# Performance work log

Hardware: AMD Instinct MI355X
Metric: run time of the kernel (lower is better)

The kernel has to match this reference:

```python
import jax, jax.numpy as jnp
import numpy as np

H_DIM = 64
GRID = 8
NS = 2.0  # neighborhood_size
S = 256   # number of sequences (scenes)
P = 64    # pedestrians per sequence
EPS = 1e-5


def setup_inputs() -> dict:
    key = jax.random.key(0)
    k = jax.random.split(key, 6)
    N = S * P
    G = GRID * GRID
    h_states = jax.random.normal(k[0], (1, N, H_DIM), jnp.float32)
    end_pos = jax.random.normal(k[1], (N, 2), jnp.float32)
    starts = (jnp.arange(S, dtype=jnp.int32) * P)
    seq_start_end = jnp.stack([starts, starts + P], axis=1)  # (S, 2)
    # mlp_pool: Linear(G*H_DIM -> H_DIM) + BatchNorm1d + ReLU
    W = jax.random.normal(k[2], (G * H_DIM, H_DIM), jnp.float32) / np.sqrt(G * H_DIM)
    b = jnp.zeros((H_DIM,), jnp.float32)
    gamma = jnp.ones((H_DIM,), jnp.float32)
    beta = jnp.zeros((H_DIM,), jnp.float32)
    return {"h_states": h_states, "seq_start_end": seq_start_end, "end_pos": end_pos,
            "W": W, "b": b, "gamma": gamma, "beta": beta}


def reference(h_states, seq_start_end, end_pos, W, b, gamma, beta):
    nseq = seq_start_end.shape[0]          # S (static)
    N = end_pos.shape[0]
    Hd = h_states.shape[-1]
    nped = N // nseq                       # P (static; equal-length sequences)
    G = GRID * GRID
    half = NS / 2.0

    h = h_states.reshape(N, Hd).reshape(nseq, nped, Hd)     # (S, P, H)
    pos = end_pos.reshape(nseq, nped, 2)                    # (S, P, 2)

    # bounds per center pedestrian i
    tl_x = pos[..., 0] - half   # (S, P)
    tl_y = pos[..., 1] + half
    br_x = pos[..., 0] + half
    br_y = pos[..., 1] - half

    # pairwise: axis 1 = center i, axis 2 = other k
    ox = pos[:, None, :, 0]     # (S, 1, P)
    oy = pos[:, None, :, 1]
    cell_x = jnp.floor((ox - tl_x[:, :, None]) / NS * GRID)
    cell_y = jnp.floor((tl_y[:, :, None] - oy) / NS * GRID)
    grid = cell_x + cell_y * GRID                            # (S, P, P)

    oob = ((ox >= br_x[:, :, None]) | (ox <= tl_x[:, :, None]) |
           (oy >= tl_y[:, :, None]) | (oy <= br_y[:, :, None]))
    diag = jnp.eye(nped, dtype=bool)[None]                   # self excluded (within_bound[0::P+1]=1)
    valid = (~oob) & (~diag)

    grid_i = jnp.clip(grid.astype(jnp.int32), 0, G - 1)      # masked entries don't matter
    seq_off = (jnp.arange(nseq, dtype=jnp.int32)[:, None, None] * nped
               + jnp.arange(nped, dtype=jnp.int32)[None, :, None]) * G
    dummy = nseq * nped * G
    ids = jnp.where(valid, seq_off + grid_i, dummy)          # (S, P, P)

    # data for (s, i, k) is hidden of other k (curr_hidden.repeat(num_ped, 1))
    data = jnp.broadcast_to(h[:, None, :, :], (nseq, nped, nped, Hd)).reshape(-1, Hd)
    pooled = jax.ops.segment_sum(data, ids.reshape(-1), num_segments=dummy + 1)[:-1]
    x = pooled.reshape(N, G * Hd)                            # (N, G*H), row i = concat over grid cells

    # mlp_pool: Linear -> BatchNorm1d (train mode, biased var) -> ReLU
    x = x @ W + b
    mu = jnp.mean(x, axis=0)
    var = jnp.mean((x - mu) ** 2, axis=0)
    x = gamma * (x - mu) / jnp.sqrt(var + EPS) + beta
    return jnp.maximum(x, 0.0)
```

## Files before the change

kernel.cpp:

```cpp
#include <hip/hip_runtime.h>
#include <hip/hip_bf16.h>


#define NSEQ 256
#define NTOT (NSEQ*64)
#define EPSV 1e-5f

typedef __attribute__((ext_vector_type(8))) short short8;
typedef __attribute__((ext_vector_type(4))) float f32x4;
typedef unsigned short ushort_t;

__device__ __forceinline__ ushort_t f2b(float f) {
    __hip_bfloat16 h = __float2bfloat16(f);
    return *reinterpret_cast<ushort_t*>(&h);
}
__device__ __forceinline__ int kperm(int k) {
    return ((k >> 5)*2 + ((k & 7) >> 2))*16 + ((k >> 3) & 3)*4 + (k & 3);
}

__global__ __launch_bounds__(256) void sp_transpose(
    const float* __restrict__ W, short* __restrict__ Wt)
{
    __shared__ __align__(16) float Tl[64*68];
    const int b = blockIdx.x, tid = threadIdx.x;
    const float* wg = W + (size_t)b*4096;
    for (int m = 0; m < 4; ++m) {
        int c = m*256 + tid;
        int k = c >> 4, t0 = (c & 15)*4;
        *(f32x4*)(Tl + k*68 + t0) = *(const f32x4*)(wg + k*64 + t0);
    }
    __syncthreads();
    for (int m = 0; m < 2; ++m) {
        int q = m*256 + tid;
        int col = q >> 3, k0 = (q & 7)*8;
        short8 o;
        #pragma unroll
        for (int i2 = 0; i2 < 8; ++i2)
            o[i2] = (short)f2b(Tl[kperm(k0 + i2)*68 + col]);
        *(short8*)(Wt + ((size_t)(b*64 + col)*64 + k0)) = o;
    }
}

#define SM_CM   9216
#define SM_POS  13312
#define SM_RED  17408
#define SM_TOT  19456

__global__ __launch_bounds__(512, 2) void sp_main(
    const float* __restrict__ h, const float* __restrict__ pos,
    const short* __restrict__ Wt, const float* __restrict__ bvec,
    float* __restrict__ X, float* __restrict__ partials)
{
    __shared__ __align__(16) char smem[SM_TOT];
    ushort_t*      Ht = (ushort_t*)(smem);
    unsigned char* cm = (unsigned char*)(smem + SM_CM);
    float*         px = (float*)(smem + SM_POS);
    float*         py = px + 64;

    const int b    = blockIdx.x;
    const int base = b * 64;
    const int tid  = threadIdx.x;
    const int lane = tid & 63, w = tid >> 6;
    const int ln15 = lane & 15, ln4 = lane >> 4;

    if (tid < 64) { px[tid] = pos[(base + tid)*2]; py[tid] = pos[(base + tid)*2 + 1]; }
    for (int m = 0; m < 2; ++m) {
        int c = m*512 + tid;
        int j = c >> 4, t0 = (c & 15)*4;
        f32x4 v = *(const f32x4*)(h + (size_t)(base + j)*64 + t0);
        #pragma unroll
        for (int u = 0; u < 4; ++u) Ht[(t0 + u)*72 + j] = f2b(v[u]);
    }
    __syncthreads();

    for (int m = 0; m < 8; ++m) {
        int p = m*512 + tid;
        int i = p >> 6, j = p & 63;
        unsigned char val = 255;
        if (i != j) {
            float ax = px[i], ay = py[i], ox = px[j], oy = py[j];
            float tlx = ax - 1.0f, tly = ay + 1.0f, brx = ax + 1.0f, bry = ay - 1.0f;
            bool oob = (ox >= brx) | (ox <= tlx) | (oy >= tly) | (oy <= bry);
            if (!oob) {
                int g = (int)(floorf((ox - tlx)*4.0f) + floorf((tly - oy)*4.0f)*8.0f);
                g = g < 0 ? 0 : (g > 63 ? 63 : g);
                val = (unsigned char)g;
            }
        }
        cm[i*64 + j] = val;
    }
    __syncthreads();

    short8 hf2[4][2];
    #pragma unroll
    for (int mt = 0; mt < 4; ++mt)
        #pragma unroll
        for (int kt2 = 0; kt2 < 2; ++kt2)
            hf2[mt][kt2] = *(const short8*)(Ht + (mt*16 + ln15)*72 + kt2*32 + ln4*8);
    unsigned cmv[4][2][2];
    #pragma unroll
    for (int rt = 0; rt < 4; ++rt)
        #pragma unroll
        for (int kt = 0; kt < 2; ++kt) {
            const unsigned* cp = (const unsigned*)(cm + (rt*16 + ln15)*64 + kt*32 + ln4*8);
            cmv[rt][kt][0] = cp[0]; cmv[rt][kt][1] = cp[1];
        }

    f32x4 acc[4][4];
    #pragma unroll
    for (int rt = 0; rt < 4; ++rt)
        #pragma unroll
        for (int nt = 0; nt < 4; ++nt) acc[rt][nt] = (f32x4){0.f,0.f,0.f,0.f};

    for (int c = 0; c < 8; ++c) {
        const int g = w*8 + ((c + b) & 7);
        const short* wg = Wt + (size_t)g*4096;
        short8 bw[2][4];
        #pragma unroll
        for (int kt = 0; kt < 2; ++kt)
            #pragma unroll
            for (int nt = 0; nt < 4; ++nt)
                bw[kt][nt] = *(const short8*)(wg + (nt*16 + ln15)*64 + kt*32 + ln4*8);

        #pragma unroll
        for (int rt = 0; rt < 4; ++rt) {
            short8 sf[2];
            #pragma unroll
            for (int kt = 0; kt < 2; ++kt)
                #pragma unroll
                for (int u = 0; u < 8; ++u) {
                    unsigned byte = ((u < 4 ? cmv[rt][kt][0] >> (8*u)
                                           : cmv[rt][kt][1] >> (8*(u-4))) & 255u);
                    sf[kt][u] = (byte == (unsigned)g) ? (short)0x3F80 : (short)0;
                }
            f32x4 pt[4];
            #pragma unroll
            for (int mt = 0; mt < 4; ++mt) pt[mt] = (f32x4){0.f,0.f,0.f,0.f};
            #pragma unroll
            for (int kt2 = 0; kt2 < 2; ++kt2)
                #pragma unroll
                for (int mt = 0; mt < 4; ++mt)
                    pt[mt] = __builtin_amdgcn_mfma_f32_16x16x32_bf16(hf2[mt][kt2], sf[kt2], pt[mt], 0, 0, 0);
            #pragma unroll
            for (int kt = 0; kt < 2; ++kt) {
                short8 af;
                #pragma unroll
                for (int r = 0; r < 4; ++r) {
                    af[r]     = (short)f2b(pt[2*kt    ][r]);
                    af[4 + r] = (short)f2b(pt[2*kt + 1][r]);
                }
                #pragma unroll
                for (int nt = 0; nt < 4; ++nt)
                    acc[rt][nt] = __builtin_amdgcn_mfma_f32_16x16x32_bf16(af, bw[kt][nt], acc[rt][nt], 0, 0, 0);
            }
        }
    }
    __syncthreads();

    float* Xs = (float*)smem;
    for (int wv = 0; wv < 8; ++wv) {
        if (w == wv) {
            #pragma unroll
            for (int rt = 0; rt < 4; ++rt)
                #pragma unroll
                for (int nt = 0; nt < 4; ++nt)
                    #pragma unroll
                    for (int r = 0; r < 4; ++r) {
                        int row = rt*16 + ln4*4 + r;
                        int col = nt*16 + ln15;
                        if (wv == 0) Xs[row*68 + col]  = acc[rt][nt][r];
                        else         Xs[row*68 + col] += acc[rt][nt][r];
                    }
        }
        __syncthreads();
    }

    {
        const int row = tid >> 3, c0 = (tid & 7)*8;
        float* xg = X + (size_t)(base + row)*64 + c0;
        #pragma unroll
        for (int q = 0; q < 2; ++q) {
            f32x4 v;
            #pragma unroll
            for (int u = 0; u < 4; ++u) v[u] = Xs[row*68 + c0 + q*4 + u] + bvec[c0 + q*4 + u];
            *(f32x4*)(xg + q*4) = v;
        }
    }

    {
        float* red1 = (float*)(smem + SM_RED);
        float* red2 = red1 + 256;
        if (tid < 256) {
            int col = tid & 63, rg = tid >> 6;
            float bc = bvec[col], s1 = 0.f, s2 = 0.f;
            for (int ii = 0; ii < 16; ++ii) {
                float xv = Xs[(rg*16 + ii)*68 + col] + bc;
                s1 += xv; s2 += xv*xv;
            }
            red1[rg*64 + col] = s1;
            red2[rg*64 + col] = s2;
        }
        __syncthreads();
        if (tid < 128) {
            int hs = tid >> 6, c2 = tid & 63;
            const float* r0 = hs ? red2 : red1;
            float v = r0[c2] + r0[64 + c2] + r0[128 + c2] + r0[192 + c2];
            partials[(size_t)b*128 + hs*64 + c2] = v;
        }
    }
}

__global__ __launch_bounds__(256) void sp_finish(
    float* __restrict__ X, const float* __restrict__ partials,
    const float* __restrict__ gamma, const float* __restrict__ beta)
{
    __shared__ float sp0[128], sp1[128];
    __shared__ float scale[64], shift[64];
    const int b = blockIdx.x, tid = threadIdx.x;

    {
        const int slot = tid & 127, hb = tid >> 7;
        float v = 0.f;
        const float* p = partials + (size_t)hb*128*128 + slot;
        #pragma unroll 4
        for (int bb = 0; bb < 128; ++bb) v += p[(size_t)bb*128];
        (hb ? sp1 : sp0)[slot] = v;
    }
    __syncthreads();
    if (tid < 64) {
        const float inv_n = 1.0f / (float)NTOT;
        float s1 = sp0[tid] + sp1[tid];
        float s2 = sp0[64 + tid] + sp1[64 + tid];
        float mu  = s1 * inv_n;
        float var = s2 * inv_n - mu*mu;
        float sc  = gamma[tid] / sqrtf(var + EPSV);
        scale[tid] = sc;
        shift[tid] = beta[tid] - mu*sc;
    }
    __syncthreads();
    #pragma unroll
    for (int q = 0; q < 4; ++q) {
        size_t idx4 = (size_t)b*1024 + q*256 + tid;
        f32x4 v = ((f32x4*)X)[idx4];
        int c0 = ((int)idx4*4) & 63;
        #pragma unroll
        for (int u = 0; u < 4; ++u)
            v[u] = fmaxf(v[u]*scale[c0 + u] + shift[c0 + u], 0.0f);
        ((f32x4*)X)[idx4] = v;
    }
}

extern "C" void kernel_launch(void* const* d_in, const int* in_sizes, int n_in,
                              void* d_out, int out_size, void* d_ws, size_t ws_size,
                              hipStream_t stream)
{
    const float* h     = (const float*)d_in[0];
    const float* pos   = (const float*)d_in[2];
    const float* W     = (const float*)d_in[3];
    const float* bvec  = (const float*)d_in[4];
    const float* gamma = (const float*)d_in[5];
    const float* beta  = (const float*)d_in[6];

    float* X        = (float*)d_out;
    short* Wt       = (short*)d_ws;
    float* partials = (float*)((char*)d_ws + 524288);

    sp_transpose<<<64,   256, 0, stream>>>(W, Wt);
    sp_main     <<<NSEQ, 512, 0, stream>>>(h, pos, Wt, bvec, X, partials);
    sp_finish   <<<NSEQ, 256, 0, stream>>>(X, partials, gamma, beta);
}
```

Before: 117.2 us.

## Double-buffer W fragment loads and halve cross-wave reduction steps

Unrolls the per-cell loop and loads the next grid cell's W fragments into a second register set while the current cell computes, so global-load latency can overlap MFMA work. The cross-wave accumulation now uses two shared-memory buffers, one per group of four waves, which cuts the serialized reduction from eight barrier steps to four. The two buffers are summed when the output is written and when the batch-norm partial sums are computed. The cell rotation phase now uses (b>>3)&7 instead of b&7. The cost is more registers for the second fragment set and about twice the LDS per block, which may affect occupancy under the 512,2 launch bound.

```diff
diff --git a/kernel.cpp b/kernel.cpp
--- a/kernel.cpp
+++ b/kernel.cpp
@@ -43,8 +43,9 @@
 
 #define SM_CM   9216
 #define SM_POS  13312
-#define SM_RED  17408
-#define SM_TOT  19456
+#define SM_XS1  17408
+#define SM_RED  34816
+#define SM_TOT  36864
 
 __global__ __launch_bounds__(512, 2) void sp_main(
     const float* __restrict__ h, const float* __restrict__ pos,
@@ -62,6 +63,7 @@
     const int tid  = threadIdx.x;
     const int lane = tid & 63, w = tid >> 6;
     const int ln15 = lane & 15, ln4 = lane >> 4;
+    const int xph  = (b >> 3) & 7;
 
     if (tid < 64) { px[tid] = pos[(base + tid)*2]; py[tid] = pos[(base + tid)*2 + 1]; }
     for (int m = 0; m < 2; ++m) {
@@ -112,16 +114,17 @@
         #pragma unroll
         for (int nt = 0; nt < 4; ++nt) acc[rt][nt] = (f32x4){0.f,0.f,0.f,0.f};
 
-    for (int c = 0; c < 8; ++c) {
-        const int g = w*8 + ((c + b) & 7);
+    auto load_cell = [&](short8 (&bw)[2][4], int cidx) {
+        const int g = w*8 + ((cidx + xph) & 7);
         const short* wg = Wt + (size_t)g*4096;
-        short8 bw[2][4];
         #pragma unroll
         for (int kt = 0; kt < 2; ++kt)
             #pragma unroll
             for (int nt = 0; nt < 4; ++nt)
                 bw[kt][nt] = *(const short8*)(wg + (nt*16 + ln15)*64 + kt*32 + ln4*8);
-
+    };
+    auto compute_cell = [&](const short8 (&bw)[2][4], int cidx) {
+        const int g = w*8 + ((cidx + xph) & 7);
         #pragma unroll
         for (int rt = 0; rt < 4; ++rt) {
             short8 sf[2];
@@ -154,12 +157,24 @@
                     acc[rt][nt] = __builtin_amdgcn_mfma_f32_16x16x32_bf16(af, bw[kt][nt], acc[rt][nt], 0, 0, 0);
             }
         }
-    }
-    __syncthreads();
-
-    float* Xs = (float*)smem;
-    for (int wv = 0; wv < 8; ++wv) {
-        if (w == wv) {
+    };
+
+    short8 bwA[2][4], bwB[2][4];
+    load_cell(bwA, 0);
+    #pragma unroll
+    for (int cc = 0; cc < 8; cc += 2) {
+        if (cc + 1 < 8) load_cell(bwB, cc + 1);
+        compute_cell(bwA, cc);
+        if (cc + 2 < 8) load_cell(bwA, cc + 2);
+        if (cc + 1 < 8) compute_cell(bwB, cc + 1);
+    }
+    __syncthreads();
+
+    float* Xs0 = (float*)smem;
+    float* Xs1 = (float*)(smem + SM_XS1);
+    for (int step = 0; step < 4; ++step) {
+        if ((w & 3) == step) {
+            float* Xs = (w < 4) ? Xs0 : Xs1;
             #pragma unroll
             for (int rt = 0; rt < 4; ++rt)
                 #pragma unroll
@@ -168,8 +183,8 @@
                     for (int r = 0; r < 4; ++r) {
                         int row = rt*16 + ln4*4 + r;
                         int col = nt*16 + ln15;
-                        if (wv == 0) Xs[row*68 + col]  = acc[rt][nt][r];
-                        else         Xs[row*68 + col] += acc[rt][nt][r];
+                        if (step == 0) Xs[row*68 + col]  = acc[rt][nt][r];
+                        else           Xs[row*68 + col] += acc[rt][nt][r];
                     }
         }
         __syncthreads();
@@ -182,7 +197,10 @@
         for (int q = 0; q < 2; ++q) {
             f32x4 v;
             #pragma unroll
-            for (int u = 0; u < 4; ++u) v[u] = Xs[row*68 + c0 + q*4 + u] + bvec[c0 + q*4 + u];
+            for (int u = 0; u < 4; ++u) {
+                int o = row*68 + c0 + q*4 + u;
+                v[u] = Xs0[o] + Xs1[o] + bvec[c0 + q*4 + u];
+            }
             *(f32x4*)(xg + q*4) = v;
         }
     }
@@ -194,7 +212,8 @@
             int col = tid & 63, rg = tid >> 6;
             float bc = bvec[col], s1 = 0.f, s2 = 0.f;
             for (int ii = 0; ii < 16; ++ii) {
-                float xv = Xs[(rg*16 + ii)*68 + col] + bc;
+                int o = (rg*16 + ii)*68 + col;
+                float xv = Xs0[o] + Xs1[o] + bc;
                 s1 += xv; s2 += xv*xv;
             }
             red1[rg*64 + col] = s1;
```

After: 104.1 us. 11.1% less time.
